# Performance work log

Hardware: AMD Instinct MI355X
Metric: run time of the kernel (lower is better)

## Reference

```python
import jax, jax.numpy as jnp
import numpy as np

EMBED_DIM = 1024
NUM_HEADS = 16
HEAD_DIM = EMBED_DIM // NUM_HEADS


def setup_inputs() -> dict:
    key = jax.random.key(0)
    ks = jax.random.split(key, 9)
    s = 1.0 / np.sqrt(EMBED_DIM)
    x = jax.random.normal(ks[0], (4, 2048, EMBED_DIM), dtype=jnp.float32)
    Wq = jax.random.uniform(ks[1], (EMBED_DIM, EMBED_DIM), jnp.float32, -s, s)
    bq = jax.random.uniform(ks[2], (EMBED_DIM,), jnp.float32, -s, s)
    Wk = jax.random.uniform(ks[3], (EMBED_DIM, EMBED_DIM), jnp.float32, -s, s)
    bk = jax.random.uniform(ks[4], (EMBED_DIM,), jnp.float32, -s, s)
    Wv = jax.random.uniform(ks[5], (EMBED_DIM, EMBED_DIM), jnp.float32, -s, s)
    bv = jax.random.uniform(ks[6], (EMBED_DIM,), jnp.float32, -s, s)
    Wo = jax.random.uniform(ks[7], (EMBED_DIM, EMBED_DIM), jnp.float32, -s, s)
    bo = jax.random.uniform(ks[8], (EMBED_DIM,), jnp.float32, -s, s)
    return {"x": x, "Wq": Wq, "bq": bq, "Wk": Wk, "bk": bk,
            "Wv": Wv, "bv": bv, "Wo": Wo, "bo": bo}


def reference(x, Wq, bq, Wk, bk, Wv, bv, Wo, bo):
    N, S, E = x.shape
    H, D = NUM_HEADS, HEAD_DIM
    # Linear projections (torch Linear: x @ W.T + b; weights here stored as [out,in])
    def proj(W, b):
        y = x @ W.T + b                      # [N,S,E]
        return y.reshape(N, S, H, D).transpose(0, 2, 1, 3)  # [N,H,S,D]
    q = proj(Wq, bq)
    k = proj(Wk, bk)
    v = proj(Wv, bv)
    energy = jnp.einsum('nhqd,nhkd->nhqk', q, k)
    attn = jax.nn.softmax(energy / jnp.sqrt(jnp.float32(D)), axis=3)
    out = jnp.einsum('nhql,nhld->nhqd', attn, v)
    out = out.transpose(0, 2, 1, 3).reshape(N, S, E)
    return out @ Wo.T + bo
```

## Files before the change

### kernel.cpp

```cpp
#include <hip/hip_runtime.h>
#include <hip/hip_bf16.h>
#include <math.h>


#define SEQ 2048
#define EMB 1024
#define NB  4
#define NH  16
#define HD  64
#define MR  (NB*SEQ)
#define NT  (SEQ/64)

typedef __attribute__((ext_vector_type(8))) short bf8;
typedef __attribute__((ext_vector_type(4))) float f4;
typedef unsigned short u16;
typedef unsigned int   u32;

#define MFMA(a,b,c) __builtin_amdgcn_mfma_f32_16x16x32_bf16(a,b,c,0,0,0)
#define QSCALE 0.180336880f

typedef __attribute__((address_space(3))) u32 lds32;
typedef const __attribute__((address_space(1))) u32 glb32;
__device__ __forceinline__ void gload16(const u16* g, u16* l) {
    __builtin_amdgcn_global_load_lds((glb32*)g, (lds32*)l, 16, 0, 0);
}

__device__ __forceinline__ u16 bf16rtn(float x) {
    u32 u = __float_as_uint(x);
    u += 0x7fff + ((u >> 16) & 1);
    return (u16)(u >> 16);
}
__device__ __forceinline__ void split1(float x, u16& h, u16& l) {
    h = bf16rtn(x);
    const float hf = __uint_as_float((u32)h << 16);
    l = bf16rtn(x - hf);
}
__device__ __forceinline__ u32 cvtpk(float a, float b) {
    union { __hip_bfloat162 v; u32 u; } t;
    t.v = __float22bfloat162_rn(float2{a, b});
    return t.u;
}

__global__ __launch_bounds__(256)
void cvt_hi(const float* __restrict__ src, u16* __restrict__ hi, int n4)
{
    int i = blockIdx.x * 256 + threadIdx.x;
    if (i >= n4) return;
    float4 f = ((const float4*)src)[i];
    ushort4 h;
    h.x = bf16rtn(f.x); h.y = bf16rtn(f.y);
    h.z = bf16rtn(f.z); h.w = bf16rtn(f.w);
    ((ushort4*)hi)[i] = h;
}

__global__ __launch_bounds__(256)
void cvt_hi4(const float* __restrict__ s0, const float* __restrict__ s1,
             const float* __restrict__ s2, const float* __restrict__ s3,
             u16* __restrict__ wsp, int n4)
{
    const int y = blockIdx.y;
    const float* src = (y == 0) ? s0 : (y == 1) ? s1 : (y == 2) ? s2 : s3;
    u16* hi = wsp + (size_t)y * (size_t)n4 * 4;
    int i = blockIdx.x * 256 + threadIdx.x;
    if (i >= n4) return;
    float4 f = ((const float4*)src)[i];
    ushort4 h;
    h.x = bf16rtn(f.x); h.y = bf16rtn(f.y);
    h.z = bf16rtn(f.z); h.w = bf16rtn(f.w);
    ((ushort4*)hi)[i] = h;
}

__global__ __launch_bounds__(256)
void gemm_qkv(const u16* __restrict__ xhi,
              const u16* __restrict__ wq, const u16* __restrict__ wk,
              const u16* __restrict__ wv,
              const float* __restrict__ bq, const float* __restrict__ bk,
              const float* __restrict__ bv,
              u16* __restrict__ Qil, u16* __restrict__ Kil,
              u16* __restrict__ Vil)
{
    __shared__ __align__(16) u16 As[128*32];
    __shared__ __align__(16) u16 Bs[128*32];

    const int z = blockIdx.z;
    const u16* Ahi  = (z == 0) ? wq : (z == 1) ? wk : xhi;
    const u16* Bhi  = (z == 2) ? wv : xhi;
    const float* bias = (z == 0) ? bq : (z == 1) ? bk : bv;
    const float scale = (z == 0) ? QSCALE : 1.0f;
    u16* Yil = (z == 0) ? Qil : (z == 1) ? Kil : Vil;

    const int t  = threadIdx.x;
    const int bm = ((z == 2) ? blockIdx.x : blockIdx.y) * 128;
    const int bn = ((z == 2) ? blockIdx.y : blockIdx.x) * 128;
    const int wv_ = t >> 6, ln = t & 63;
    const int wr = wv_ >> 1, wc = wv_ & 1;
    const int r  = ln & 15, g = ln >> 4;

    const int scol8 = (ln & 3) ^ ((ln >> 3) & 3);

    f4 acc[4][4];
#pragma unroll
    for (int i = 0; i < 4; ++i)
#pragma unroll
        for (int j = 0; j < 4; ++j)
#pragma unroll
            for (int e = 0; e < 4; ++e) acc[i][j][e] = 0.f;

    for (int k0 = 0; k0 < EMB; k0 += 32) {
        __syncthreads();
#pragma unroll
        for (int q = 0; q < 2; ++q) {
            const int chunk = q*4 + wv_;
            const int row = chunk*16 + (ln >> 2);
            gload16(&Ahi[(size_t)(bm+row)*EMB + k0 + scol8*8], &As[chunk*512]);
            gload16(&Bhi[(size_t)(bn+row)*EMB + k0 + scol8*8], &Bs[chunk*512]);
        }
        __syncthreads();

        const int cA = (g ^ ((r >> 1) & 3)) << 3;
        bf8 ah[4];
#pragma unroll
        for (int mi = 0; mi < 4; ++mi)
            ah[mi] = *(const bf8*)&As[(wr*64 + mi*16 + r)*32 + cA];
#pragma unroll
        for (int ni = 0; ni < 4; ++ni) {
            const bf8 bh = *(const bf8*)&Bs[(wc*64 + ni*16 + r)*32 + cA];
#pragma unroll
            for (int mi = 0; mi < 4; ++mi)
                acc[mi][ni] = MFMA(ah[mi], bh, acc[mi][ni]);
        }
    }

#pragma unroll
    for (int mi = 0; mi < 4; ++mi) {
        const int m0 = bm + wr*64 + mi*16 + g*4;
#pragma unroll
        for (int ni = 0; ni < 4; ++ni) {
            const int n0 = bn + wc*64 + ni*16 + r;
            if (z != 2) {
                const float4 b4 = *(const float4*)&bias[m0];
                const int h = m0 >> 6, d = m0 & (HD-1);
                const int nn = n0 >> 11, s = n0 & (SEQ-1);
                const size_t base = (((size_t)nn*NH + h)*SEQ + s)*(2*HD) + d;
                ushort4 hh;
                hh.x = bf16rtn((acc[mi][ni][0] + b4.x) * scale);
                hh.y = bf16rtn((acc[mi][ni][1] + b4.y) * scale);
                hh.z = bf16rtn((acc[mi][ni][2] + b4.z) * scale);
                hh.w = bf16rtn((acc[mi][ni][3] + b4.w) * scale);
                *(ushort4*)&Yil[base] = hh;
            } else {
                const float b = bias[n0];
                const int nn = m0 >> 11, s = m0 & (SEQ-1);
                const int h = n0 >> 6, d = n0 & (HD-1);
                const size_t base = (((size_t)nn*NH + h)*HD + d)*(2*SEQ) + s;
                ushort4 hh;
                hh.x = bf16rtn(acc[mi][ni][0] + b);
                hh.y = bf16rtn(acc[mi][ni][1] + b);
                hh.z = bf16rtn(acc[mi][ni][2] + b);
                hh.w = bf16rtn(acc[mi][ni][3] + b);
                *(ushort4*)&Yil[base] = hh;
            }
        }
    }
}

__global__ __launch_bounds__(256)
void gemm_final(const u16* __restrict__ Ahi,
                const u16* __restrict__ Bhi, const u16* __restrict__ Blo,
                const float* __restrict__ bias, float* __restrict__ Yf)
{
    __shared__ __align__(16) u16 As[128*32];
    __shared__ __align__(16) u16 Bs0[128*32];
    __shared__ __align__(16) u16 Bs1[128*32];

    const int t  = threadIdx.x;
    const int bm = blockIdx.y * 128, bn = blockIdx.x * 128;
    const int wv_ = t >> 6, ln = t & 63;
    const int wr = wv_ >> 1, wc = wv_ & 1;
    const int r  = ln & 15, g = ln >> 4;

    const int scol8 = (ln & 3) ^ ((ln >> 3) & 3);

    f4 acc[4][4];
#pragma unroll
    for (int i = 0; i < 4; ++i)
#pragma unroll
        for (int j = 0; j < 4; ++j)
#pragma unroll
            for (int e = 0; e < 4; ++e) acc[i][j][e] = 0.f;

    for (int k0 = 0; k0 < EMB; k0 += 32) {
        __syncthreads();
#pragma unroll
        for (int q = 0; q < 2; ++q) {
            const int chunk = q*4 + wv_;
            const int row = chunk*16 + (ln >> 2);
            const size_t ga = (size_t)(bm+row)*EMB + k0 + scol8*8;
            const size_t gb = (size_t)(bn+row)*EMB + k0 + scol8*8;
            gload16(&Ahi[ga], &As [chunk*512]);
            gload16(&Bhi[gb], &Bs0[chunk*512]);
            gload16(&Blo[gb], &Bs1[chunk*512]);
        }
        __syncthreads();

        const int cA = (g ^ ((r >> 1) & 3)) << 3;
        bf8 ah[4];
#pragma unroll
        for (int mi = 0; mi < 4; ++mi)
            ah[mi] = *(const bf8*)&As[(wr*64 + mi*16 + r)*32 + cA];
#pragma unroll
        for (int ni = 0; ni < 4; ++ni) {
            const int off = (wc*64 + ni*16 + r)*32 + cA;
            const bf8 bh = *(const bf8*)&Bs0[off];
            const bf8 bl = *(const bf8*)&Bs1[off];
#pragma unroll
            for (int mi = 0; mi < 4; ++mi) {
                acc[mi][ni] = MFMA(ah[mi], bl, acc[mi][ni]);
                acc[mi][ni] = MFMA(ah[mi], bh, acc[mi][ni]);
            }
        }
    }

#pragma unroll
    for (int mi = 0; mi < 4; ++mi) {
        const int m0 = bm + wr*64 + mi*16 + g*4;
#pragma unroll
        for (int ni = 0; ni < 4; ++ni) {
            const int n0 = bn + wc*64 + ni*16 + r;
            const float4 b4 = *(const float4*)&bias[m0];
            float4 o;
            o.x = acc[mi][ni][0] + b4.x; o.y = acc[mi][ni][1] + b4.y;
            o.z = acc[mi][ni][2] + b4.z; o.w = acc[mi][ni][3] + b4.w;
            *(float4*)&Yf[(size_t)n0*EMB + m0] = o;
        }
    }
}

#define LDSRD(arr,row,col) (*(const bf8*)((const char*)(arr) + \
        ((((row)<<7) | ((col)<<1)) ^ (((row)&7)<<4))))

__global__ __launch_bounds__(512)
void attn_mfma(const u16* __restrict__ Qil, const u16* __restrict__ Kil,
               const u16* __restrict__ Vil,
               u16* __restrict__ Ohi, u16* __restrict__ Olo)
{
    __shared__ __align__(16) u16 KH[2][64*64];
    __shared__ __align__(16) u16 VH[2][64*64];
    __shared__ __align__(16) u16 Ps[8*32*64];

    const int t = threadIdx.x, w = t >> 6, lane = t & 63;
    const int r = lane & 15, g = lane >> 4;
    const int wg = blockIdx.x;
    const int nh = (wg & 7) | ((wg >> 6) << 3);
    const int qb = (wg >> 3) & 7;
    const int qw = qb * 256 + w * 32;
    const u16* Qb = Qil + (size_t)nh * SEQ * 2*HD;
    const u16* Kb = Kil + (size_t)nh * SEQ * 2*HD;
    const u16* Vb = Vil + (size_t)nh * HD * 2*SEQ;
    u16* Pw = &Ps[w * 32 * 64];

    bf8 ones8;
#pragma unroll
    for (int i = 0; i < 8; ++i) ones8[i] = (short)0x3F80;

    bf8 qh[2][2];
#pragma unroll
    for (int mi = 0; mi < 2; ++mi)
#pragma unroll
        for (int c = 0; c < 2; ++c) {
            const size_t off = (size_t)(qw + mi*16 + r)*(2*HD) + c*32 + g*8;
            qh[mi][c] = *(const bf8*)&Qb[off];
        }

    f4 oacc[2][4];
    f4 lacc[2];
#pragma unroll
    for (int mi = 0; mi < 2; ++mi) {
#pragma unroll
        for (int e = 0; e < 4; ++e) lacc[mi][e] = 0.f;
#pragma unroll
        for (int df = 0; df < 4; ++df)
#pragma unroll
            for (int e = 0; e < 4; ++e) oacc[mi][df][e] = 0.f;
    }

    const int srow = t >> 3, sc8 = (t & 7) * 8;
    const int soff = ((srow << 7) | (sc8 << 1)) ^ ((srow & 7) << 4);

    uint4 kh_r, vh_r;
    kh_r = *(const uint4*)&Kb[(size_t)srow*(2*HD) + sc8];
    vh_r = *(const uint4*)&Vb[(size_t)srow*(2*SEQ) + sc8];
    *(uint4*)((char*)&KH[0][0] + soff) = kh_r;
    *(uint4*)((char*)&VH[0][0] + soff) = vh_r;
    {
        const int ktn = (NT > 1) ? 1 : 0;
        kh_r = *(const uint4*)&Kb[(size_t)(ktn*64 + srow)*(2*HD) + sc8];
        vh_r = *(const uint4*)&Vb[(size_t)srow*(2*SEQ) + ktn*64 + sc8];
    }
    __syncthreads();

    for (int kt = 0; kt < NT; ++kt) {
        const int cur = kt & 1;
        const u16* KHc = &KH[cur][0];
        const u16* VHc = &VH[cur][0];

        f4 s[2][4];
#pragma unroll
        for (int mi = 0; mi < 2; ++mi)
#pragma unroll
            for (int kf = 0; kf < 4; ++kf)
#pragma unroll
                for (int e = 0; e < 4; ++e) s[mi][kf][e] = 0.f;
#pragma unroll
        for (int kf = 0; kf < 4; ++kf) {
#pragma unroll
            for (int c = 0; c < 2; ++c) {
                const int col = c*32 + g*8;
                const bf8 kh = LDSRD(KHc, kf*16 + r, col);
#pragma unroll
                for (int mi = 0; mi < 2; ++mi)
                    s[mi][kf] = MFMA(kh, qh[mi][c], s[mi][kf]);
            }
        }

#pragma unroll
        for (int mi = 0; mi < 2; ++mi)
#pragma unroll
            for (int kf = 0; kf < 4; ++kf) {
                uint2 v2;
                v2.x = cvtpk(exp2f(s[mi][kf][0]), exp2f(s[mi][kf][1]));
                v2.y = cvtpk(exp2f(s[mi][kf][2]), exp2f(s[mi][kf][3]));
                const int row = mi*16 + r, col = kf*16 + g*4;
                *(uint2*)((char*)Pw + (((row<<7) | (col<<1)) ^ ((row&7)<<4))) = v2;
            }

#pragma unroll
        for (int c = 0; c < 2; ++c) {
            const int col = c*32 + g*8;
            bf8 pa[2];
#pragma unroll
            for (int mi = 0; mi < 2; ++mi) {
                pa[mi] = LDSRD(Pw, mi*16 + r, col);
                lacc[mi] = MFMA(ones8, pa[mi], lacc[mi]);
            }
#pragma unroll
            for (int df = 0; df < 4; ++df) {
                const bf8 vh = LDSRD(VHc, df*16 + r, col);
#pragma unroll
                for (int mi = 0; mi < 2; ++mi)
                    oacc[mi][df] = MFMA(vh, pa[mi], oacc[mi][df]);
            }
        }

        *(uint4*)((char*)&KH[cur ^ 1][0] + soff) = kh_r;
        *(uint4*)((char*)&VH[cur ^ 1][0] + soff) = vh_r;
        {
            const int ktn = (kt + 2 < NT) ? kt + 2 : NT - 1;
            kh_r = *(const uint4*)&Kb[(size_t)(ktn*64 + srow)*(2*HD) + sc8];
            vh_r = *(const uint4*)&Vb[(size_t)srow*(2*SEQ) + ktn*64 + sc8];
        }
        __syncthreads();
    }

    const int n = nh >> 4, h = nh & 15;
#pragma unroll
    for (int mi = 0; mi < 2; ++mi) {
        const float inv = 1.0f / lacc[mi][0];
        const int q = qw + mi*16 + r;
        const size_t base = ((size_t)n*SEQ + q)*EMB + h*HD;
#pragma unroll
        for (int df = 0; df < 4; ++df) {
            ushort4 hh, ll;
            split1(oacc[mi][df][0] * inv, hh.x, ll.x);
            split1(oacc[mi][df][1] * inv, hh.y, ll.y);
            split1(oacc[mi][df][2] * inv, hh.z, ll.z);
            split1(oacc[mi][df][3] * inv, hh.w, ll.w);
            *(ushort4*)&Ohi[base + df*16 + g*4] = hh;
            *(ushort4*)&Olo[base + df*16 + g*4] = ll;
        }
    }
}

extern "C" void kernel_launch(void* const* d_in, const int* in_sizes, int n_in,
                              void* d_out, int out_size, void* d_ws, size_t ws_size,
                              hipStream_t stream)
{
    const float* x  = (const float*)d_in[0];
    const float* Wq = (const float*)d_in[1];
    const float* bq = (const float*)d_in[2];
    const float* Wk = (const float*)d_in[3];
    const float* bk = (const float*)d_in[4];
    const float* Wv = (const float*)d_in[5];
    const float* bv = (const float*)d_in[6];
    const float* Wo = (const float*)d_in[7];
    const float* bo = (const float*)d_in[8];

    const size_t MB = (size_t)1 << 20;
    char* W = (char*)d_ws;
    u16* xhi = (u16*)(W + 0);
    u16* olo = (u16*)(W + 16*MB);
    u16* wsp = (u16*)(W + 32*MB);
    u16* Qil = (u16*)(W + 48*MB);
    u16* Kil = (u16*)(W + 80*MB);
    u16* Vil = (u16*)(W + 112*MB);
    const size_t WN = 1048576;
    u16 *wqh = wsp, *wkh = wsp + WN, *wvh = wsp + 2*WN, *woh = wsp + 3*WN;
    u16 *ohi = xhi;

    cvt_hi<<<dim3(MR*EMB/4/256), dim3(256), 0, stream>>>(x, xhi, MR*EMB/4);
    cvt_hi4<<<dim3(WN/4/256, 4), dim3(256), 0, stream>>>(Wq, Wk, Wv, Wo, wsp, WN/4);

    gemm_qkv<<<dim3(MR/128, EMB/128, 3), dim3(256), 0, stream>>>(
        xhi, wqh, wkh, wvh, bq, bk, bv, Qil, Kil, Vil);

    attn_mfma<<<dim3(SEQ/256 * NB*NH), dim3(512), 0, stream>>>(Qil, Kil, Vil, ohi, olo);

    gemm_final<<<dim3(MR/128, EMB/128), dim3(256), 0, stream>>>(
        woh, ohi, olo, bo, (float*)d_out);
}
```

Before: 268.6 us.

## Double GEMM K-tile depth, merge conversion kernels, reorder attention loop and use fast exp2

```diff
diff --git a/kernel.cpp b/kernel.cpp
--- a/kernel.cpp
+++ b/kernel.cpp
@@ -19,6 +19,16 @@
 #define MFMA(a,b,c) __builtin_amdgcn_mfma_f32_16x16x32_bf16(a,b,c,0,0,0)
 #define QSCALE 0.180336880f
 
+#if defined(__has_builtin)
+#if __has_builtin(__builtin_amdgcn_exp2f)
+#define EXP2(x) __builtin_amdgcn_exp2f(x)
+#else
+#define EXP2(x) exp2f(x)
+#endif
+#else
+#define EXP2(x) exp2f(x)
+#endif
+
 typedef __attribute__((address_space(3))) u32 lds32;
 typedef const __attribute__((address_space(1))) u32 glb32;
 __device__ __forceinline__ void gload16(const u16* g, u16* l) {
@@ -41,33 +51,29 @@
     return t.u;
 }
 
+#define X4 (MR*EMB/4)
+#define W4 (EMB*EMB/4)
 __global__ __launch_bounds__(256)
-void cvt_hi(const float* __restrict__ src, u16* __restrict__ hi, int n4)
+void cvt_all(const float* __restrict__ x,
+             const float* __restrict__ q0, const float* __restrict__ q1,
+             const float* __restrict__ q2, const float* __restrict__ q3,
+             u16* __restrict__ xhi, u16* __restrict__ wsp)
 {
-    int i = blockIdx.x * 256 + threadIdx.x;
-    if (i >= n4) return;
-    float4 f = ((const float4*)src)[i];
+    const int id = blockIdx.x * 256 + threadIdx.x;
+    const float* src; u16* dst; int idx;
+    if (id < X4) { src = x; dst = xhi; idx = id; }
+    else {
+        const int j = id - X4;
+        const int y = j >> 18;
+        idx = j & (W4 - 1);
+        src = (y == 0) ? q0 : (y == 1) ? q1 : (y == 2) ? q2 : q3;
+        dst = wsp + (size_t)y * (EMB*(size_t)EMB);
+    }
+    float4 f = ((const float4*)src)[idx];
     ushort4 h;
     h.x = bf16rtn(f.x); h.y = bf16rtn(f.y);
     h.z = bf16rtn(f.z); h.w = bf16rtn(f.w);
-    ((ushort4*)hi)[i] = h;
-}
-
-__global__ __launch_bounds__(256)
-void cvt_hi4(const float* __restrict__ s0, const float* __restrict__ s1,
-             const float* __restrict__ s2, const float* __restrict__ s3,
-             u16* __restrict__ wsp, int n4)
-{
-    const int y = blockIdx.y;
-    const float* src = (y == 0) ? s0 : (y == 1) ? s1 : (y == 2) ? s2 : s3;
-    u16* hi = wsp + (size_t)y * (size_t)n4 * 4;
-    int i = blockIdx.x * 256 + threadIdx.x;
-    if (i >= n4) return;
-    float4 f = ((const float4*)src)[i];
-    ushort4 h;
-    h.x = bf16rtn(f.x); h.y = bf16rtn(f.y);
-    h.z = bf16rtn(f.z); h.w = bf16rtn(f.w);
-    ((ushort4*)hi)[i] = h;
+    ((ushort4*)dst)[idx] = h;
 }
 
 __global__ __launch_bounds__(256)
@@ -79,8 +85,8 @@
               u16* __restrict__ Qil, u16* __restrict__ Kil,
               u16* __restrict__ Vil)
 {
-    __shared__ __align__(16) u16 As[128*32];
-    __shared__ __align__(16) u16 Bs[128*32];
+    __shared__ __align__(16) u16 As[128*64];
+    __shared__ __align__(16) u16 Bs[128*64];
 
     const int z = blockIdx.z;
     const u16* Ahi  = (z == 0) ? wq : (z == 1) ? wk : xhi;
@@ -92,11 +98,11 @@
     const int t  = threadIdx.x;
     const int bm = ((z == 2) ? blockIdx.x : blockIdx.y) * 128;
     const int bn = ((z == 2) ? blockIdx.y : blockIdx.x) * 128;
-    const int wv_ = t >> 6, ln = t & 63;
-    const int wr = wv_ >> 1, wc = wv_ & 1;
+    const int wid = t >> 6, ln = t & 63;
+    const int wr = wid >> 1, wc = wid & 1;
     const int r  = ln & 15, g = ln >> 4;
 
-    const int scol8 = (ln & 3) ^ ((ln >> 3) & 3);
+    const int scol8 = (ln & 7) ^ ((ln >> 3) & 7);
 
     f4 acc[4][4];
 #pragma unroll
@@ -106,28 +112,31 @@
 #pragma unroll
             for (int e = 0; e < 4; ++e) acc[i][j][e] = 0.f;
 
-    for (int k0 = 0; k0 < EMB; k0 += 32) {
+    for (int k0 = 0; k0 < EMB; k0 += 64) {
         __syncthreads();
 #pragma unroll
-        for (int q = 0; q < 2; ++q) {
-            const int chunk = q*4 + wv_;
-            const int row = chunk*16 + (ln >> 2);
+        for (int is = 0; is < 4; ++is) {
+            const int chunk = is*4 + wid;
+            const int row = chunk*8 + (ln >> 3);
             gload16(&Ahi[(size_t)(bm+row)*EMB + k0 + scol8*8], &As[chunk*512]);
             gload16(&Bhi[(size_t)(bn+row)*EMB + k0 + scol8*8], &Bs[chunk*512]);
         }
         __syncthreads();
 
-        const int cA = (g ^ ((r >> 1) & 3)) << 3;
-        bf8 ah[4];
-#pragma unroll
-        for (int mi = 0; mi < 4; ++mi)
-            ah[mi] = *(const bf8*)&As[(wr*64 + mi*16 + r)*32 + cA];
-#pragma unroll
-        for (int ni = 0; ni < 4; ++ni) {
-            const bf8 bh = *(const bf8*)&Bs[(wc*64 + ni*16 + r)*32 + cA];
+#pragma unroll
+        for (int kk = 0; kk < 2; ++kk) {
+            const int cA = ((kk*4 + g) ^ (r & 7)) << 3;
+            bf8 ah[4];
 #pragma unroll
             for (int mi = 0; mi < 4; ++mi)
-                acc[mi][ni] = MFMA(ah[mi], bh, acc[mi][ni]);
+                ah[mi] = *(const bf8*)&As[(wr*64 + mi*16 + r)*64 + cA];
+#pragma unroll
+            for (int ni = 0; ni < 4; ++ni) {
+                const bf8 bh = *(const bf8*)&Bs[(wc*64 + ni*16 + r)*64 + cA];
+#pragma unroll
+                for (int mi = 0; mi < 4; ++mi)
+                    acc[mi][ni] = MFMA(ah[mi], bh, acc[mi][ni]);
+            }
         }
     }
 
@@ -169,17 +178,17 @@
                 const u16* __restrict__ Bhi, const u16* __restrict__ Blo,
                 const float* __restrict__ bias, float* __restrict__ Yf)
 {
-    __shared__ __align__(16) u16 As[128*32];
-    __shared__ __align__(16) u16 Bs0[128*32];
-    __shared__ __align__(16) u16 Bs1[128*32];
+    __shared__ __align__(16) u16 As[128*64];
+    __shared__ __align__(16) u16 Bs0[128*64];
+    __shared__ __align__(16) u16 Bs1[128*64];
 
     const int t  = threadIdx.x;
     const int bm = blockIdx.y * 128, bn = blockIdx.x * 128;
-    const int wv_ = t >> 6, ln = t & 63;
-    const int wr = wv_ >> 1, wc = wv_ & 1;
+    const int wid = t >> 6, ln = t & 63;
+    const int wr = wid >> 1, wc = wid & 1;
     const int r  = ln & 15, g = ln >> 4;
 
-    const int scol8 = (ln & 3) ^ ((ln >> 3) & 3);
+    const int scol8 = (ln & 7) ^ ((ln >> 3) & 7);
 
     f4 acc[4][4];
 #pragma unroll
@@ -189,12 +198,12 @@
 #pragma unroll
             for (int e = 0; e < 4; ++e) acc[i][j][e] = 0.f;
 
-    for (int k0 = 0; k0 < EMB; k0 += 32) {
+    for (int k0 = 0; k0 < EMB; k0 += 64) {
         __syncthreads();
 #pragma unroll
-        for (int q = 0; q < 2; ++q) {
-            const int chunk = q*4 + wv_;
-            const int row = chunk*16 + (ln >> 2);
+        for (int is = 0; is < 4; ++is) {
+            const int chunk = is*4 + wid;
+            const int row = chunk*8 + (ln >> 3);
             const size_t ga = (size_t)(bm+row)*EMB + k0 + scol8*8;
             const size_t gb = (size_t)(bn+row)*EMB + k0 + scol8*8;
             gload16(&Ahi[ga], &As [chunk*512]);
@@ -203,20 +212,23 @@
         }
         __syncthreads();
 
-        const int cA = (g ^ ((r >> 1) & 3)) << 3;
-        bf8 ah[4];
-#pragma unroll
-        for (int mi = 0; mi < 4; ++mi)
-            ah[mi] = *(const bf8*)&As[(wr*64 + mi*16 + r)*32 + cA];
-#pragma unroll
-        for (int ni = 0; ni < 4; ++ni) {
-            const int off = (wc*64 + ni*16 + r)*32 + cA;
-            const bf8 bh = *(const bf8*)&Bs0[off];
-            const bf8 bl = *(const bf8*)&Bs1[off];
-#pragma unroll
-            for (int mi = 0; mi < 4; ++mi) {
-                acc[mi][ni] = MFMA(ah[mi], bl, acc[mi][ni]);
-                acc[mi][ni] = MFMA(ah[mi], bh, acc[mi][ni]);
+#pragma unroll
+        for (int kk = 0; kk < 2; ++kk) {
+            const int cA = ((kk*4 + g) ^ (r & 7)) << 3;
+            bf8 ah[4];
+#pragma unroll
+            for (int mi = 0; mi < 4; ++mi)
+                ah[mi] = *(const bf8*)&As[(wr*64 + mi*16 + r)*64 + cA];
+#pragma unroll
+            for (int ni = 0; ni < 4; ++ni) {
+                const int off = (wc*64 + ni*16 + r)*64 + cA;
+                const bf8 bh = *(const bf8*)&Bs0[off];
+                const bf8 bl = *(const bf8*)&Bs1[off];
+#pragma unroll
+                for (int mi = 0; mi < 4; ++mi) {
+                    acc[mi][ni] = MFMA(ah[mi], bl, acc[mi][ni]);
+                    acc[mi][ni] = MFMA(ah[mi], bh, acc[mi][ni]);
+                }
             }
         }
     }
@@ -323,35 +335,6 @@
             }
         }
 
-#pragma unroll
-        for (int mi = 0; mi < 2; ++mi)
-#pragma unroll
-            for (int kf = 0; kf < 4; ++kf) {
-                uint2 v2;
-                v2.x = cvtpk(exp2f(s[mi][kf][0]), exp2f(s[mi][kf][1]));
-                v2.y = cvtpk(exp2f(s[mi][kf][2]), exp2f(s[mi][kf][3]));
-                const int row = mi*16 + r, col = kf*16 + g*4;
-                *(uint2*)((char*)Pw + (((row<<7) | (col<<1)) ^ ((row&7)<<4))) = v2;
-            }
-
-#pragma unroll
-        for (int c = 0; c < 2; ++c) {
-            const int col = c*32 + g*8;
-            bf8 pa[2];
-#pragma unroll
-            for (int mi = 0; mi < 2; ++mi) {
-                pa[mi] = LDSRD(Pw, mi*16 + r, col);
-                lacc[mi] = MFMA(ones8, pa[mi], lacc[mi]);
-            }
-#pragma unroll
-            for (int df = 0; df < 4; ++df) {
-                const bf8 vh = LDSRD(VHc, df*16 + r, col);
-#pragma unroll
-                for (int mi = 0; mi < 2; ++mi)
-                    oacc[mi][df] = MFMA(vh, pa[mi], oacc[mi][df]);
-            }
-        }
-
         *(uint4*)((char*)&KH[cur ^ 1][0] + soff) = kh_r;
         *(uint4*)((char*)&VH[cur ^ 1][0] + soff) = vh_r;
         {
@@ -359,6 +342,36 @@
             kh_r = *(const uint4*)&Kb[(size_t)(ktn*64 + srow)*(2*HD) + sc8];
             vh_r = *(const uint4*)&Vb[(size_t)srow*(2*SEQ) + ktn*64 + sc8];
         }
+
+#pragma unroll
+        for (int mi = 0; mi < 2; ++mi)
+#pragma unroll
+            for (int kf = 0; kf < 4; ++kf) {
+                uint2 v2;
+                v2.x = cvtpk(EXP2(s[mi][kf][0]), EXP2(s[mi][kf][1]));
+                v2.y = cvtpk(EXP2(s[mi][kf][2]), EXP2(s[mi][kf][3]));
+                const int row = mi*16 + r, col = kf*16 + g*4;
+                *(uint2*)((char*)Pw + (((row<<7) | (col<<1)) ^ ((row&7)<<4))) = v2;
+            }
+
+#pragma unroll
+        for (int c = 0; c < 2; ++c) {
+            const int col = c*32 + g*8;
+            bf8 pa[2];
+#pragma unroll
+            for (int mi = 0; mi < 2; ++mi) {
+                pa[mi] = LDSRD(Pw, mi*16 + r, col);
+                lacc[mi] = MFMA(ones8, pa[mi], lacc[mi]);
+            }
+#pragma unroll
+            for (int df = 0; df < 4; ++df) {
+                const bf8 vh = LDSRD(VHc, df*16 + r, col);
+#pragma unroll
+                for (int mi = 0; mi < 2; ++mi)
+                    oacc[mi][df] = MFMA(vh, pa[mi], oacc[mi][df]);
+            }
+        }
+
         __syncthreads();
     }
 
@@ -407,8 +420,8 @@
     u16 *wqh = wsp, *wkh = wsp + WN, *wvh = wsp + 2*WN, *woh = wsp + 3*WN;
     u16 *ohi = xhi;
 
-    cvt_hi<<<dim3(MR*EMB/4/256), dim3(256), 0, stream>>>(x, xhi, MR*EMB/4);
-    cvt_hi4<<<dim3(WN/4/256, 4), dim3(256), 0, stream>>>(Wq, Wk, Wv, Wo, wsp, WN/4);
+    cvt_all<<<dim3((X4 + 4*W4)/256), dim3(256), 0, stream>>>(
+        x, Wq, Wk, Wv, Wo, xhi, wsp);
 
     gemm_qkv<<<dim3(MR/128, EMB/128, 3), dim3(256), 0, stream>>>(
         xhi, wqh, wkh, wvh, bq, bk, bv, Qil, Kil, Vil);
```

After: 231.4 us (median of 2 runs). 1.16x faster.
